# Kernel tuning notes

Hardware: AMD Instinct MI355X
Metric: run time of the kernel (lower is better)

## Reference

```python
import jax, jax.numpy as jnp
import numpy as np


def _highpass_coeffs(filter_freq, filter_q, sample_rate):
    # torchaudio.functional.highpass_biquad coefficient formulas
    w0 = 2.0 * jnp.pi * filter_freq[0] / sample_rate
    alpha = jnp.sin(w0) / (2.0 * filter_q[0])
    cosw0 = jnp.cos(w0)
    b0 = (1.0 + cosw0) / 2.0
    b1 = -(1.0 + cosw0)
    b2 = b0
    a0 = 1.0 + alpha
    a1 = -2.0 * cosw0
    a2 = 1.0 - alpha
    # normalize by a0 (as lfilter does)
    return b0 / a0, b1 / a0, b2 / a0, a1 / a0, a2 / a0


def _biquad(x, b0, b1, b2, a1, a2):
    # x: [B, T]; sequential direct-form-I IIR over the time axis
    B = x.shape[0]
    xt = jnp.swapaxes(x, 0, 1)  # [T, B]

    def step(carry, x_t):
        x1, x2, y1, y2 = carry
        y_t = b0 * x_t + b1 * x1 + b2 * x2 - a1 * y1 - a2 * y2
        return (x_t, x1, y_t, y1), y_t

    z = jnp.zeros((B,), dtype=x.dtype)
    _, yt = jax.lax.scan(step, (z, z, z, z), xt)
    return jnp.swapaxes(yt, 0, 1)  # [B, T]


def setup_inputs() -> dict:
    key = jax.random.key(0)
    k1, = jax.random.split(key, 1)
    B, T = 64, 524288
    x = jax.random.normal(k1, (B, T), dtype=jnp.float32)
    filter_freq = jnp.array([1500.0], dtype=jnp.float32)
    filter_q = jnp.array([0.9], dtype=jnp.float32)
    return {"x": x, "filter_freq": filter_freq, "filter_q": filter_q, "sample_rate": 44100}


def reference(x, filter_freq, filter_q, sample_rate):
    b0, b1, b2, a1, a2 = _highpass_coeffs(filter_freq.astype(x.dtype), filter_q.astype(x.dtype), sample_rate)
    return _biquad(x, b0, b1, b2, a1, a2)
```

## Files before the change

### kernel.cpp

```cpp
#include <hip/hip_runtime.h>
#include <math.h>


typedef float f4 __attribute__((ext_vector_type(4)));

namespace {
constexpr int T_LEN = 524288;
constexpr int B_ROWS = 64;
constexpr int LT = 256;
constexpr int WU = 128;
constexpr int CPR = T_LEN / LT;
constexpr int NV = T_LEN / 4;
constexpr int STRIDEV = LT / 4;
constexpr int ITERS = (WU + LT) / 32;
constexpr int SKIP = WU / 32;
}

using gfp = const float __attribute__((address_space(1)))*;
using lfp = float __attribute__((address_space(3)))*;

__global__ __launch_bounds__(64) void hp_biquad(
    const float* __restrict__ x,
    const float* __restrict__ ffreq,
    const float* __restrict__ fqv,
    const int*  __restrict__ srv,
    float* __restrict__ y)
{
    __shared__ f4 inb[2][512];
    __shared__ f4 outb[512];

    const float fsr   = (float)srv[0];
    const float w0    = 6.28318530717958647692f * ffreq[0] / fsr;
    const float sw    = sinf(w0);
    const float cw    = cosf(w0);
    const float alpha = sw / (2.0f * fqv[0]);
    const float ia0   = 1.0f / (1.0f + alpha);
    const float b0 = 0.5f * (1.0f + cw) * ia0;
    const float b1 = -(1.0f + cw) * ia0;
    const float b2 = b0;
    const float a1 = -2.0f * cw * ia0;
    const float a2 = (1.0f - alpha) * ia0;

    const int lane = threadIdx.x;
    const int wv   = blockIdx.x;
    const int c0   = wv * 64;
    const int row  = c0 / CPR;
    const int c0r  = c0 & (CPR - 1);
    const bool firstWave  = (c0r == 0);
    const int rowBaseVec  = row * NV;
    const int waveVecBase = rowBaseVec + c0r * STRIDEV - WU / 4;

    const int vstar   = (lane & 7) ^ ((lane >> 3) & 7);
    const int laneOff = (lane >> 3) * STRIDEV + vstar;

    const f4* __restrict__ xv = (const f4*)x;
    f4* __restrict__ yv       = (f4*)y;

    auto issue_loads = [&](int k, int bufi) {
        const int base  = waveVecBase + 8 * k + laneOff;
        const bool clmp = firstWave && (k < SKIP);
#pragma unroll
        for (int j = 0; j < 8; ++j) {
            int idx = base + j * (8 * STRIDEV);
            if (clmp) idx = idx < rowBaseVec ? rowBaseVec : idx;
            __builtin_amdgcn_global_load_lds(
                (gfp)(const float*)(xv + idx),
                (lfp)(float*)(&inb[bufi][j * 64]), 16, 0, 0);
        }
    };

    float xm1 = 0.f, xm2 = 0.f, ym1 = 0.f, ym2 = 0.f;
    auto step = [&](float xt) -> float {
        float t  = b0 * xt + b1 * xm1 + b2 * xm2 - a2 * ym2;
        float yt = t - a1 * ym1;
        xm2 = xm1; xm1 = xt;
        ym2 = ym1; ym1 = yt;
        return yt;
    };

    issue_loads(0, 0);

    for (int k = 0; k < ITERS; ++k) {
        const int bufi = k & 1;
        if (k + 1 < ITERS) issue_loads(k + 1, bufi ^ 1);

        if (k > SKIP && k + 1 < ITERS) {
            asm volatile("s_waitcnt vmcnt(16)" ::: "memory");
        } else {
            asm volatile("s_waitcnt vmcnt(8)" ::: "memory");
        }
        __builtin_amdgcn_sched_barrier(0);

        f4 r[8];
#pragma unroll
        for (int v = 0; v < 8; ++v)
            r[v] = inb[bufi][(lane << 3) + (v ^ (lane & 7))];

        if (firstWave && lane == 0 && k < SKIP) {
#pragma unroll
            for (int v = 0; v < 8; ++v) r[v] = (f4)(0.f);
        }

        f4 o[8];
#pragma unroll
        for (int v = 0; v < 8; ++v) {
            o[v].x = step(r[v].x);
            o[v].y = step(r[v].y);
            o[v].z = step(r[v].z);
            o[v].w = step(r[v].w);
        }

        if (k >= SKIP) {
#pragma unroll
            for (int v = 0; v < 8; ++v)
                outb[(lane << 3) + (v ^ (lane & 7))] = o[v];
            f4 t[8];
#pragma unroll
            for (int j = 0; j < 8; ++j)
                t[j] = outb[(j << 6) + lane];
            const int obase = waveVecBase + 8 * k + laneOff;
#pragma unroll
            for (int j = 0; j < 8; ++j)
                yv[obase + j * (8 * STRIDEV)] = t[j];
        }
    }
}

extern "C" void kernel_launch(void* const* d_in, const int* in_sizes, int n_in,
                              void* d_out, int out_size, void* d_ws, size_t ws_size,
                              hipStream_t stream) {
    const float* x  = (const float*)d_in[0];
    const float* ff = (const float*)d_in[1];
    const float* fq = (const float*)d_in[2];
    const int*   sr = (const int*)d_in[3];
    float* out = (float*)d_out;

    const int grid  = (B_ROWS * CPR) / 64;
    const int block = 64;
    hp_biquad<<<grid, block, 0, stream>>>(x, ff, fq, sr, out);
}
```

Before: 56.10 us.

## Double chunk length and per-iteration vector group, reuse input LDS as output staging

```diff
diff --git a/kernel.cpp b/kernel.cpp
--- a/kernel.cpp
+++ b/kernel.cpp
@@ -7,13 +7,14 @@
 namespace {
 constexpr int T_LEN = 524288;
 constexpr int B_ROWS = 64;
-constexpr int LT = 256;
+constexpr int LT = 512;
 constexpr int WU = 128;
 constexpr int CPR = T_LEN / LT;
 constexpr int NV = T_LEN / 4;
 constexpr int STRIDEV = LT / 4;
-constexpr int ITERS = (WU + LT) / 32;
-constexpr int SKIP = WU / 32;
+constexpr int GV = 16;
+constexpr int ITERS = (WU + LT) / (4 * GV);
+constexpr int SKIP = WU / (4 * GV);
 }
 
 using gfp = const float __attribute__((address_space(1)))*;
@@ -26,8 +27,7 @@
     const int*  __restrict__ srv,
     float* __restrict__ y)
 {
-    __shared__ f4 inb[2][512];
-    __shared__ f4 outb[512];
+    __shared__ f4 inb[2][1024];
 
     const float fsr   = (float)srv[0];
     const float w0    = 6.28318530717958647692f * ffreq[0] / fsr;
@@ -50,18 +50,20 @@
     const int rowBaseVec  = row * NV;
     const int waveVecBase = rowBaseVec + c0r * STRIDEV - WU / 4;
 
-    const int vstar   = (lane & 7) ^ ((lane >> 3) & 7);
-    const int laneOff = (lane >> 3) * STRIDEV + vstar;
+    const int sub = (lane >> 4) * STRIDEV;
+    const int ve  = (lane & 15) ^ (lane >> 4);
+    const int laneOffE = sub + ve;
+    const int laneOffO = sub + (ve ^ 4);
 
     const f4* __restrict__ xv = (const f4*)x;
     f4* __restrict__ yv       = (f4*)y;
 
     auto issue_loads = [&](int k, int bufi) {
-        const int base  = waveVecBase + 8 * k + laneOff;
+        const int base  = waveVecBase + GV * k;
         const bool clmp = firstWave && (k < SKIP);
 #pragma unroll
-        for (int j = 0; j < 8; ++j) {
-            int idx = base + j * (8 * STRIDEV);
+        for (int j = 0; j < 16; ++j) {
+            int idx = base + j * (4 * STRIDEV) + ((j & 1) ? laneOffO : laneOffE);
             if (clmp) idx = idx < rowBaseVec ? rowBaseVec : idx;
             __builtin_amdgcn_global_load_lds(
                 (gfp)(const float*)(xv + idx),
@@ -84,26 +86,26 @@
         const int bufi = k & 1;
         if (k + 1 < ITERS) issue_loads(k + 1, bufi ^ 1);
 
-        if (k > SKIP && k + 1 < ITERS) {
+        if (k >= 3 && k <= 8) {
+            asm volatile("s_waitcnt vmcnt(32)" ::: "memory");
+        } else {
             asm volatile("s_waitcnt vmcnt(16)" ::: "memory");
-        } else {
-            asm volatile("s_waitcnt vmcnt(8)" ::: "memory");
         }
         __builtin_amdgcn_sched_barrier(0);
 
-        f4 r[8];
+        f4 r[GV];
 #pragma unroll
-        for (int v = 0; v < 8; ++v)
-            r[v] = inb[bufi][(lane << 3) + (v ^ (lane & 7))];
+        for (int v = 0; v < GV; ++v)
+            r[v] = inb[bufi][(lane << 4) + (v ^ (lane & 7))];
 
         if (firstWave && lane == 0 && k < SKIP) {
 #pragma unroll
-            for (int v = 0; v < 8; ++v) r[v] = (f4)(0.f);
+            for (int v = 0; v < GV; ++v) r[v] = (f4)(0.f);
         }
 
-        f4 o[8];
+        f4 o[GV];
 #pragma unroll
-        for (int v = 0; v < 8; ++v) {
+        for (int v = 0; v < GV; ++v) {
             o[v].x = step(r[v].x);
             o[v].y = step(r[v].y);
             o[v].z = step(r[v].z);
@@ -112,16 +114,16 @@
 
         if (k >= SKIP) {
 #pragma unroll
-            for (int v = 0; v < 8; ++v)
-                outb[(lane << 3) + (v ^ (lane & 7))] = o[v];
-            f4 t[8];
+            for (int v = 0; v < GV; ++v)
+                inb[bufi][(lane << 4) + (v ^ (lane & 7))] = o[v];
+            f4 t[16];
 #pragma unroll
-            for (int j = 0; j < 8; ++j)
-                t[j] = outb[(j << 6) + lane];
-            const int obase = waveVecBase + 8 * k + laneOff;
+            for (int j = 0; j < 16; ++j)
+                t[j] = inb[bufi][(j << 6) + lane];
+            const int obase = waveVecBase + GV * k;
 #pragma unroll
-            for (int j = 0; j < 8; ++j)
-                yv[obase + j * (8 * STRIDEV)] = t[j];
+            for (int j = 0; j < 16; ++j)
+                yv[obase + j * (4 * STRIDEV) + ((j & 1) ? laneOffO : laneOffE)] = t[j];
         }
     }
 }
```

New measurement: 49.09 us. 12.5% less time.
